# Performance work log

Hardware: AMD Instinct MI355X
Metric: run time of the kernel (lower is better)

Reference implementation:

```python
import jax, jax.numpy as jnp
import numpy as np

N = 10000       # n_nodes
E = 640000      # n_edges (avg degree 64)
D_IN = 128      # in_feats
D_H = 128       # n_hidden
N_CLS = 64      # n_classes


def setup_inputs() -> dict:
    key = jax.random.key(0)
    k1, k2, k3, k4, k5, k6 = jax.random.split(key, 6)
    features = jax.random.normal(k1, (N, D_IN), dtype=jnp.float32)
    src = jax.random.randint(k2, (E,), 0, N, dtype=jnp.int32)
    dst = jax.random.randint(k3, (E,), 0, N, dtype=jnp.int32)
    s = 0.05  # small init scale to keep activations bounded across 3 layers
    # Stored as [in, out]; equivalent to torch Linear weight [out, in] transposed.
    W0 = jax.random.normal(k4, (D_IN, D_H), dtype=jnp.float32) * s
    W1 = jax.random.normal(k5, (D_H, D_H), dtype=jnp.float32) * s
    W2 = jax.random.normal(k6, (D_H, N_CLS), dtype=jnp.float32) * s
    return {"features": features, "W0": W0, "W1": W1, "W2": W2,
            "src": src, "dst": dst}


def reference(features, W0, W1, W2, src, dst):
    # GINConv with aggregator 'sum', eps=0 (learn_eps=False):
    #   h' = Linear(h + sum_{(u->v) in E} h[u] scattered to v)
    # Dropout is identity at inference; 'activation' is unused in the module.
    def gin_layer(h, W):
        agg = jax.ops.segment_sum(h[src], dst, num_segments=N)  # [N, d]
        return (h + agg) @ W

    h = gin_layer(features, W0)
    h = gin_layer(h, W1)
    h = gin_layer(h, W2)
    return h
```

## Files before the change

### kernel.cpp

```cpp
#include <hip/hip_runtime.h>
#include <hip/hip_bf16.h>

#define NN 10000
#define NE 640000
#define D_IN 128
#define D_H 128
#define N_CLS 64
#define CAP 160
#define GRP 157
#define CAPC 4800
#define CCS 16
#define SENT 10000
#define EPB 1024
#define AB 625
#define CB 1251
#define WB 80

__device__ __forceinline__ float blo(unsigned u) { return __uint_as_float(u << 16); }
__device__ __forceinline__ float bhi(unsigned u) { return __uint_as_float(u & 0xffff0000u); }
__device__ __forceinline__ unsigned short f2bf(float f) {
    unsigned u = __float_as_uint(f);
    return (unsigned short)((u + 0x7fffu + ((u >> 16) & 1u)) >> 16);
}
__device__ __forceinline__ unsigned packbf(float a, float b) {
    return (unsigned)f2bf(a) | ((unsigned)f2bf(b) << 16);
}

__global__ __launch_bounds__(256) void prep_a(const int* __restrict__ src,
                                              const int* __restrict__ dst,
                                              int* __restrict__ coarse_cnt,
                                              unsigned* __restrict__ coarse,
                                              const float* __restrict__ feat,
                                              unsigned* __restrict__ hb0,
                                              const float* __restrict__ W0,
                                              const float* __restrict__ W1,
                                              const float* __restrict__ W2,
                                              unsigned* __restrict__ wb0,
                                              unsigned* __restrict__ wb1,
                                              unsigned* __restrict__ wb2) {
    int bid = blockIdx.x;
    if (bid >= AB + CB) {
        int t = (bid - AB - CB) * 256 + threadIdx.x;
        if (t < 8192) {
            int kp = t >> 7, j = t & 127;
            wb0[t] = packbf(W0[(2 * kp) * 128 + j], W0[(2 * kp + 1) * 128 + j]);
        } else if (t < 16384) {
            int tt = t - 8192, kp = tt >> 7, j = tt & 127;
            wb1[tt] = packbf(W1[(2 * kp) * 128 + j], W1[(2 * kp + 1) * 128 + j]);
        } else if (t < 20480) {
            int tt = t - 16384, kp = tt >> 6, j = tt & 63;
            wb2[tt] = packbf(W2[(2 * kp) * 64 + j], W2[(2 * kp + 1) * 64 + j]);
        }
        return;
    }
    if (bid >= AB) {
        int t = (bid - AB) * 256 + threadIdx.x;
        if (t < NN * 32) {
            float4 f = ((const float4*)feat)[t];
            ((uint2*)hb0)[t] = make_uint2(packbf(f.x, f.y), packbf(f.z, f.w));
        } else if (t < (NN + 1) * 32) {
            ((uint2*)hb0)[t] = make_uint2(0u, 0u);
        }
        return;
    }
    __shared__ unsigned stage[EPB];
    __shared__ int hist[GRP], gbase[GRP], cur[GRP];
    const int t = threadIdx.x;
    for (int i = t; i < GRP; i += 256) hist[i] = 0;
    __syncthreads();
    const int e0 = bid * EPB;
    for (int i = t; i < EPB; i += 256) {
        int s = src[e0 + i];
        int d = dst[e0 + i];
        stage[i] = (unsigned)s | ((unsigned)d << 16);
        atomicAdd(&hist[d >> 6], 1);
    }
    __syncthreads();
    for (int i = t; i < GRP; i += 256) {
        gbase[i] = atomicAdd(&coarse_cnt[i * CCS], hist[i]);
        cur[i] = 0;
    }
    __syncthreads();
    for (int i = t; i < EPB; i += 256) {
        unsigned u = stage[i];
        int g = u >> 22;
        int r = atomicAdd(&cur[g], 1);
        coarse[g * CAPC + gbase[g] + r] = u;
    }
}

__global__ __launch_bounds__(1024) void prep_b(const int* __restrict__ coarse_cnt,
                                               const unsigned* __restrict__ coarse,
                                               int* __restrict__ cnt,
                                               unsigned short* __restrict__ colbuf) {
    __shared__ int cur[64];
    const int g = blockIdx.x;
    const int t = threadIdx.x;
    if (t < 64) cur[t] = 0;
    __syncthreads();
    const int m = coarse_cnt[g * CCS];
    const unsigned* cb = coarse + g * CAPC;
    for (int i = t; i < m; i += 1024) {
        unsigned u = cb[i];
        int s = (int)(u & 0xFFFFu);
        int d = (int)(u >> 16);
        int r = atomicAdd(&cur[d - (g << 6)], 1);
        colbuf[d * CAP + r] = (unsigned short)s;
    }
    __syncthreads();
    if (t < 64) {
        int n = (g << 6) + t;
        if (n < NN) {
            int c = cur[t];
            int pad = (16 - (c & 15)) & 15;
            unsigned short* base = colbuf + n * CAP;
            for (int k = 0; k < pad; ++k) base[c + k] = (unsigned short)SENT;
            cnt[n] = c + pad;
        }
    }
}

template <int J, bool LAST>
__global__ __launch_bounds__(256, 4) void gin_layer(const uint4* __restrict__ hb4,
                                                    const int* __restrict__ cnt,
                                                    const unsigned short* __restrict__ colbuf,
                                                    const unsigned* __restrict__ Wb,
                                                    unsigned short* __restrict__ outb,
                                                    float* __restrict__ outf) {
    constexpr int M = 4;
    __shared__ float xs[M][D_H];
    const int base = blockIdx.x * M;
    const int tid = threadIdx.x;
    const int wave = tid >> 6;
    const int lane = tid & 63;
    const int sub = lane >> 4;
    const int off = lane & 15;

    const int n = __builtin_amdgcn_readfirstlane(base + wave);
    float a0, a1, a2, a3, a4, a5, a6, a7;
    if (sub == 0) {
        uint4 u = hb4[n * 16 + off];
        a0 = blo(u.x); a1 = bhi(u.x); a2 = blo(u.y); a3 = bhi(u.y);
        a4 = blo(u.z); a5 = bhi(u.z); a6 = blo(u.w); a7 = bhi(u.w);
    } else {
        a0 = a1 = a2 = a3 = a4 = a5 = a6 = a7 = 0.f;
    }
    const int G4 = __builtin_amdgcn_readfirstlane(cnt[n]) >> 2;
    const uint2* cl8 = (const uint2*)(colbuf + n * CAP);
    for (int g = 0; g < G4; g += 4) {
        uint2 p0 = cl8[g + 0];
        uint2 p1 = cl8[g + 1];
        uint2 p2 = cl8[g + 2];
        uint2 p3 = cl8[g + 3];
        unsigned w0 = (sub & 2) ? p0.y : p0.x;
        unsigned w1 = (sub & 2) ? p1.y : p1.x;
        unsigned w2 = (sub & 2) ? p2.y : p2.x;
        unsigned w3 = (sub & 2) ? p3.y : p3.x;
        int s0 = (sub & 1) ? (w0 >> 16) : (w0 & 0xffffu);
        int s1 = (sub & 1) ? (w1 >> 16) : (w1 & 0xffffu);
        int s2 = (sub & 1) ? (w2 >> 16) : (w2 & 0xffffu);
        int s3 = (sub & 1) ? (w3 >> 16) : (w3 & 0xffffu);
        uint4 uA = hb4[s0 * 16 + off];
        uint4 uB = hb4[s1 * 16 + off];
        uint4 uC = hb4[s2 * 16 + off];
        uint4 uD = hb4[s3 * 16 + off];
        a0 += (blo(uA.x) + blo(uB.x)) + (blo(uC.x) + blo(uD.x));
        a1 += (bhi(uA.x) + bhi(uB.x)) + (bhi(uC.x) + bhi(uD.x));
        a2 += (blo(uA.y) + blo(uB.y)) + (blo(uC.y) + blo(uD.y));
        a3 += (bhi(uA.y) + bhi(uB.y)) + (bhi(uC.y) + bhi(uD.y));
        a4 += (blo(uA.z) + blo(uB.z)) + (blo(uC.z) + blo(uD.z));
        a5 += (bhi(uA.z) + bhi(uB.z)) + (bhi(uC.z) + bhi(uD.z));
        a6 += (blo(uA.w) + blo(uB.w)) + (blo(uC.w) + blo(uD.w));
        a7 += (bhi(uA.w) + bhi(uB.w)) + (bhi(uC.w) + bhi(uD.w));
    }
    a0 += __shfl_xor(a0, 16); a0 += __shfl_xor(a0, 32);
    a1 += __shfl_xor(a1, 16); a1 += __shfl_xor(a1, 32);
    a2 += __shfl_xor(a2, 16); a2 += __shfl_xor(a2, 32);
    a3 += __shfl_xor(a3, 16); a3 += __shfl_xor(a3, 32);
    a4 += __shfl_xor(a4, 16); a4 += __shfl_xor(a4, 32);
    a5 += __shfl_xor(a5, 16); a5 += __shfl_xor(a5, 32);
    a6 += __shfl_xor(a6, 16); a6 += __shfl_xor(a6, 32);
    a7 += __shfl_xor(a7, 16); a7 += __shfl_xor(a7, 32);
    if (sub == 0) {
        *(float4*)&xs[wave][8 * off]     = make_float4(a0, a1, a2, a3);
        *(float4*)&xs[wave][8 * off + 4] = make_float4(a4, a5, a6, a7);
    }
    __syncthreads();

    constexpr int G = 256 / J;
    constexpr int NM = M / G;
    const int gq = tid / J;
    const int j = tid % J;
    const int mbase = gq * NM;
    float acc[NM];
#pragma unroll
    for (int m = 0; m < NM; ++m) acc[m] = 0.f;
    for (int k = 0; k < D_H; k += 4) {
        unsigned wp0 = Wb[(k >> 1) * J + j];
        unsigned wp1 = Wb[((k >> 1) + 1) * J + j];
        float w0 = blo(wp0), w1 = bhi(wp0), w2 = blo(wp1), w3 = bhi(wp1);
#pragma unroll
        for (int m = 0; m < NM; ++m) {
            float4 xv = *(const float4*)&xs[mbase + m][k];
            acc[m] += xv.x * w0 + xv.y * w1 + xv.z * w2 + xv.w * w3;
        }
    }
#pragma unroll
    for (int m = 0; m < NM; ++m) {
        int n2 = base + mbase + m;
        if (LAST) __builtin_nontemporal_store(acc[m], &outf[(size_t)n2 * J + j]);
        else      __builtin_nontemporal_store(f2bf(acc[m]), &outb[(size_t)n2 * J + j]);
    }
    if (!LAST && blockIdx.x == 0 && tid < 32) {
        ((uint2*)(outb + (size_t)SENT * D_H))[tid] = make_uint2(0u, 0u);
    }
}

extern "C" void kernel_launch(void* const* d_in, const int* in_sizes, int n_in,
                              void* d_out, int out_size, void* d_ws, size_t ws_size,
                              hipStream_t stream) {
    const float* feat = (const float*)d_in[0];
    const float* W0   = (const float*)d_in[1];
    const float* W1   = (const float*)d_in[2];
    const float* W2   = (const float*)d_in[3];
    const int*   src  = (const int*)d_in[4];
    const int*   dst  = (const int*)d_in[5];
    float* out = (float*)d_out;

    int* coarse_cnt        = (int*)d_ws;
    int* cnt               = coarse_cnt + GRP * CCS;
    unsigned short* colbuf = (unsigned short*)(cnt + NN + 8);
    unsigned* coarse       = (unsigned*)(colbuf + (size_t)NN * CAP);
    unsigned* hb0          = coarse + (size_t)GRP * CAPC;
    unsigned* hb1          = hb0 + (size_t)(NN + 1) * 64;
    unsigned* hb2          = hb1 + (size_t)(NN + 1) * 64;
    unsigned* wb0          = hb2 + (size_t)(NN + 1) * 64;
    unsigned* wb1          = wb0 + 8192;
    unsigned* wb2          = wb1 + 8192;

    hipMemsetAsync(coarse_cnt, 0, GRP * CCS * sizeof(int), stream);
    prep_a<<<AB + CB + WB, 256, 0, stream>>>(src, dst, coarse_cnt, coarse, feat, hb0,
                                             W0, W1, W2, wb0, wb1, wb2);
    prep_b<<<GRP, 1024, 0, stream>>>(coarse_cnt, coarse, cnt, colbuf);

    gin_layer<D_H, false><<<NN / 4, 256, 0, stream>>>((const uint4*)hb0, cnt, colbuf, wb0,
                                                      (unsigned short*)hb1, nullptr);
    gin_layer<D_H, false><<<NN / 4, 256, 0, stream>>>((const uint4*)hb1, cnt, colbuf, wb1,
                                                      (unsigned short*)hb2, nullptr);
    gin_layer<N_CLS, true><<<NN / 4, 256, 0, stream>>>((const uint4*)hb2, cnt, colbuf, wb2,
                                                       nullptr, out);
}
```

Before: 145.5 us.

## Stage CSR rows in LDS, pad to 32, unroll gather 8-wide with prefetched indices

prep_b now builds each block's 64 adjacency rows in shared memory and writes them to global with coalesced 16-byte stores, replacing scattered 2-byte global writes. Rows are padded to a multiple of 32 with sentinel entries. The aggregation loop now handles 32 neighbours per iteration, issues 8 row gathers at once, and prefetches the next chunk's indices during the accumulation, giving more memory-level parallelism. In exchange, larger padding adds sentinel gathers, the prefetch reads one chunk past the end (still inside CAP only if the count stays at or below 128), and register pressure rises.

```diff
diff --git a/kernel.cpp b/kernel.cpp
--- a/kernel.cpp
+++ b/kernel.cpp
@@ -94,6 +94,7 @@
                                                int* __restrict__ cnt,
                                                unsigned short* __restrict__ colbuf) {
     __shared__ int cur[64];
+    __shared__ unsigned short sbuf[64][CAP];
     const int g = blockIdx.x;
     const int t = threadIdx.x;
     if (t < 64) cur[t] = 0;
@@ -103,20 +104,26 @@
     for (int i = t; i < m; i += 1024) {
         unsigned u = cb[i];
         int s = (int)(u & 0xFFFFu);
-        int d = (int)(u >> 16);
-        int r = atomicAdd(&cur[d - (g << 6)], 1);
-        colbuf[d * CAP + r] = (unsigned short)s;
+        int dl = (int)(u >> 16) - (g << 6);
+        int r = atomicAdd(&cur[dl], 1);
+        sbuf[dl][r] = (unsigned short)s;
     }
     __syncthreads();
     if (t < 64) {
         int n = (g << 6) + t;
         if (n < NN) {
             int c = cur[t];
-            int pad = (16 - (c & 15)) & 15;
-            unsigned short* base = colbuf + n * CAP;
-            for (int k = 0; k < pad; ++k) base[c + k] = (unsigned short)SENT;
+            int pad = (32 - (c & 31)) & 31;
+            for (int k = 0; k < pad; ++k) sbuf[t][c + k] = (unsigned short)SENT;
             cnt[n] = c + pad;
         }
+    }
+    __syncthreads();
+    const uint4* s4 = (const uint4*)sbuf;
+    for (int idx = t; idx < 64 * (CAP / 8); idx += 1024) {
+        int node = (g << 6) + (idx / (CAP / 8));
+        if (node < NN)
+            ((uint4*)colbuf)[(size_t)node * (CAP / 8) + (idx % (CAP / 8))] = s4[idx];
     }
 }
 
@@ -145,33 +152,57 @@
     } else {
         a0 = a1 = a2 = a3 = a4 = a5 = a6 = a7 = 0.f;
     }
-    const int G4 = __builtin_amdgcn_readfirstlane(cnt[n]) >> 2;
-    const uint2* cl8 = (const uint2*)(colbuf + n * CAP);
-    for (int g = 0; g < G4; g += 4) {
-        uint2 p0 = cl8[g + 0];
-        uint2 p1 = cl8[g + 1];
-        uint2 p2 = cl8[g + 2];
-        uint2 p3 = cl8[g + 3];
+    const int NCH = __builtin_amdgcn_readfirstlane(cnt[n]) >> 5;
+    const uint2* cl = (const uint2*)(colbuf + n * CAP);
+    const int sh = (sub & 1) << 4;
+    uint2 p0 = cl[0], p1 = cl[1], p2 = cl[2], p3 = cl[3];
+    uint2 p4 = cl[4], p5 = cl[5], p6 = cl[6], p7 = cl[7];
+    for (int c = 0; c < NCH; ++c) {
         unsigned w0 = (sub & 2) ? p0.y : p0.x;
         unsigned w1 = (sub & 2) ? p1.y : p1.x;
         unsigned w2 = (sub & 2) ? p2.y : p2.x;
         unsigned w3 = (sub & 2) ? p3.y : p3.x;
-        int s0 = (sub & 1) ? (w0 >> 16) : (w0 & 0xffffu);
-        int s1 = (sub & 1) ? (w1 >> 16) : (w1 & 0xffffu);
-        int s2 = (sub & 1) ? (w2 >> 16) : (w2 & 0xffffu);
-        int s3 = (sub & 1) ? (w3 >> 16) : (w3 & 0xffffu);
-        uint4 uA = hb4[s0 * 16 + off];
-        uint4 uB = hb4[s1 * 16 + off];
-        uint4 uC = hb4[s2 * 16 + off];
-        uint4 uD = hb4[s3 * 16 + off];
-        a0 += (blo(uA.x) + blo(uB.x)) + (blo(uC.x) + blo(uD.x));
-        a1 += (bhi(uA.x) + bhi(uB.x)) + (bhi(uC.x) + bhi(uD.x));
-        a2 += (blo(uA.y) + blo(uB.y)) + (blo(uC.y) + blo(uD.y));
-        a3 += (bhi(uA.y) + bhi(uB.y)) + (bhi(uC.y) + bhi(uD.y));
-        a4 += (blo(uA.z) + blo(uB.z)) + (blo(uC.z) + blo(uD.z));
-        a5 += (bhi(uA.z) + bhi(uB.z)) + (bhi(uC.z) + bhi(uD.z));
-        a6 += (blo(uA.w) + blo(uB.w)) + (blo(uC.w) + blo(uD.w));
-        a7 += (bhi(uA.w) + bhi(uB.w)) + (bhi(uC.w) + bhi(uD.w));
+        unsigned w4 = (sub & 2) ? p4.y : p4.x;
+        unsigned w5 = (sub & 2) ? p5.y : p5.x;
+        unsigned w6 = (sub & 2) ? p6.y : p6.x;
+        unsigned w7 = (sub & 2) ? p7.y : p7.x;
+        int s0 = (int)((w0 >> sh) & 0xffffu);
+        int s1 = (int)((w1 >> sh) & 0xffffu);
+        int s2 = (int)((w2 >> sh) & 0xffffu);
+        int s3 = (int)((w3 >> sh) & 0xffffu);
+        int s4 = (int)((w4 >> sh) & 0xffffu);
+        int s5 = (int)((w5 >> sh) & 0xffffu);
+        int s6 = (int)((w6 >> sh) & 0xffffu);
+        int s7 = (int)((w7 >> sh) & 0xffffu);
+        uint4 u0 = hb4[s0 * 16 + off];
+        uint4 u1 = hb4[s1 * 16 + off];
+        uint4 u2 = hb4[s2 * 16 + off];
+        uint4 u3 = hb4[s3 * 16 + off];
+        uint4 u4 = hb4[s4 * 16 + off];
+        uint4 u5 = hb4[s5 * 16 + off];
+        uint4 u6 = hb4[s6 * 16 + off];
+        uint4 u7 = hb4[s7 * 16 + off];
+        {
+            const uint2* nx = cl + 8 * (c + 1);
+            p0 = nx[0]; p1 = nx[1]; p2 = nx[2]; p3 = nx[3];
+            p4 = nx[4]; p5 = nx[5]; p6 = nx[6]; p7 = nx[7];
+        }
+        a0 += ((blo(u0.x) + blo(u1.x)) + (blo(u2.x) + blo(u3.x)))
+            + ((blo(u4.x) + blo(u5.x)) + (blo(u6.x) + blo(u7.x)));
+        a1 += ((bhi(u0.x) + bhi(u1.x)) + (bhi(u2.x) + bhi(u3.x)))
+            + ((bhi(u4.x) + bhi(u5.x)) + (bhi(u6.x) + bhi(u7.x)));
+        a2 += ((blo(u0.y) + blo(u1.y)) + (blo(u2.y) + blo(u3.y)))
+            + ((blo(u4.y) + blo(u5.y)) + (blo(u6.y) + blo(u7.y)));
+        a3 += ((bhi(u0.y) + bhi(u1.y)) + (bhi(u2.y) + bhi(u3.y)))
+            + ((bhi(u4.y) + bhi(u5.y)) + (bhi(u6.y) + bhi(u7.y)));
+        a4 += ((blo(u0.z) + blo(u1.z)) + (blo(u2.z) + blo(u3.z)))
+            + ((blo(u4.z) + blo(u5.z)) + (blo(u6.z) + blo(u7.z)));
+        a5 += ((bhi(u0.z) + bhi(u1.z)) + (bhi(u2.z) + bhi(u3.z)))
+            + ((bhi(u4.z) + bhi(u5.z)) + (bhi(u6.z) + bhi(u7.z)));
+        a6 += ((blo(u0.w) + blo(u1.w)) + (blo(u2.w) + blo(u3.w)))
+            + ((blo(u4.w) + blo(u5.w)) + (blo(u6.w) + blo(u7.w)));
+        a7 += ((bhi(u0.w) + bhi(u1.w)) + (bhi(u2.w) + bhi(u3.w)))
+            + ((bhi(u4.w) + bhi(u5.w)) + (bhi(u6.w) + bhi(u7.w)));
     }
     a0 += __shfl_xor(a0, 16); a0 += __shfl_xor(a0, 32);
     a1 += __shfl_xor(a1, 16); a1 += __shfl_xor(a1, 32);
```

Result: no change. 147.2 us (+1.1%).
